# Optimization experiments

Hardware: AMD Instinct MI355X
Metric: run time of the kernel (lower is better)

Reference implementation:

```python
import jax, jax.numpy as jnp
import numpy as np

B, F, E = 16384, 50, 64          # batch, field_size, embedding_size
V, D = 100000, 512               # feature_size, deep_init_size
H1, H2 = 1024, 512               # deep_layers
BN_EPS = 1e-10


def setup_inputs() -> dict:
    key = jax.random.key(0)
    ks = jax.random.split(key, 14)
    g0 = np.sqrt(6.0 / (D + H1))
    g1 = np.sqrt(6.0 / (H1 + H2))
    go = np.sqrt(5.0 / (D + 1))
    return {
        "feat_index": jax.random.randint(ks[0], (B, F), 0, V),
        "feat_value": jax.random.uniform(ks[1], (B, F), dtype=jnp.float32),
        "feature_embeddings": jax.random.normal(ks[2], (V, E), dtype=jnp.float32) * 0.01,
        "product_linear": jax.random.normal(ks[3], (D, F, E), dtype=jnp.float32) * 0.01,
        "product_bias": jax.random.normal(ks[4], (D,), dtype=jnp.float32),
        "product_quadratic_inner": jax.random.normal(ks[5], (D, F), dtype=jnp.float32) * 0.01,
        "layer_0": jax.random.uniform(ks[6], (D, H1), minval=-g0, maxval=g0, dtype=jnp.float32),
        "bias_0": jax.random.uniform(ks[7], (1, H1), minval=-g0, maxval=g0, dtype=jnp.float32),
        "layer_1": jax.random.uniform(ks[8], (H1, H2), minval=-g1, maxval=g1, dtype=jnp.float32),
        "bias_1": jax.random.uniform(ks[9], (1, H2), minval=-g1, maxval=g1, dtype=jnp.float32),
        "bn_scale": jax.random.normal(ks[10], (1,), dtype=jnp.float32) * 0.01,
        "bn_offset": jax.random.normal(ks[11], (1,), dtype=jnp.float32) * 0.01,
        "output_w": jax.random.uniform(ks[12], (H2, 1), minval=-go, maxval=go, dtype=jnp.float32),
        "output_b": jnp.float32(0.01),
    }


def reference(feat_index, feat_value, feature_embeddings, product_linear,
              product_bias, product_quadratic_inner, layer_0, bias_0,
              layer_1, bias_1, bn_scale, bn_offset, output_w, output_b):
    # embedding lookup scaled by feature values: (B, F, E)
    emb = feature_embeddings[feat_index] * feat_value[..., None]
    # linear product signal: sum over field+embed dims for each of D units
    lz = jnp.einsum('bfe,dfe->bd', emb, product_linear)          # (B, D)
    # inner quadratic signal: field-weighted sum then L2 norm over embed dim
    s = jnp.einsum('bfe,df->bde', emb, product_quadratic_inner)  # (B, D, E)
    lp = jnp.sqrt(jnp.sum(s * s, axis=-1))                       # (B, D)
    y = jax.nn.relu(lz + lp + product_bias)
    # dropout omitted (deterministic eval-mode reference)
    for W, bvec in ((layer_0, bias_0), (layer_1, bias_1)):
        y = y @ W + bvec
        m = jnp.mean(y, axis=0)
        v = jnp.var(y, axis=0)
        y = (y - m) * jax.lax.rsqrt(v + BN_EPS) * bn_scale + bn_offset
        y = jax.nn.relu(y)
    out = y @ output_w + output_b
    return jax.nn.sigmoid(out)
```

## Files before the change

### kernel.cpp

```cpp
#include <hip/hip_runtime.h>

typedef unsigned short u16;
typedef __attribute__((ext_vector_type(8))) short bf16x8v;
typedef __attribute__((ext_vector_type(4))) float f32x4v;

#define B_SZ 16384
#define F_SZ 50
#define E_SZ 64
#define D_SZ 512
#define H1_SZ 1024
#define H2_SZ 512
#define KL 3200
#define KG 1280

__device__ __forceinline__ float b2f(u16 u){
  union { unsigned int i; float f; } v; v.i = ((unsigned int)u) << 16; return v.f;
}
__device__ __forceinline__ u16 f2b(float f){
  union { float f; unsigned int i; } v; v.f = f;
  unsigned int r = v.i + 0x7FFFu + ((v.i >> 16) & 1u);
  return (u16)(r >> 16);
}

__device__ __forceinline__ void gload16(const u16* g, u16* lds_base_uniform){
#if __has_builtin(__builtin_amdgcn_global_load_lds)
  __builtin_amdgcn_global_load_lds(
      (const __attribute__((address_space(1))) unsigned int*)g,
      (__attribute__((address_space(3))) unsigned int*)lds_base_uniform,
      16, 0, 0);
#else
  int lane = threadIdx.x & 63;
  *(uint4*)(lds_base_uniform + lane*8) = *(const uint4*)g;
#endif
}

__device__ __forceinline__ void swz(int id, int nblog2, int &x, int &y){
  int xcd = id & 7, j = id >> 3;
  x = j & ((1 << nblog2) - 1);
  y = ((j >> nblog2) << 3) | xcd;
}

__global__ __launch_bounds__(256) void k_gather(
    const int* __restrict__ fidx, const float* __restrict__ fval,
    const float* __restrict__ femb, u16* __restrict__ embT,
    u16* __restrict__ Gp)
{
  __shared__ int   sidx[F_SZ];
  __shared__ float sfv[F_SZ];
  __shared__ __align__(16) u16 tile[64*72];
  const int b = blockIdx.x, t = threadIdx.x;
  const int wave = t >> 6, lane = t & 63, quad = lane >> 4, l16 = lane & 15;
  if (t < F_SZ){ sidx[t] = fidx[b*F_SZ+t]; sfv[t] = fval[b*F_SZ+t]; }
  __syncthreads();
  #pragma unroll
  for (int i=0;i<4;i++){
    int k4 = (i*256+t)*4;
    if (k4 < F_SZ*E_SZ){
      int f = k4>>6, e = k4&63;
      float4 v = *(const float4*)&femb[(size_t)sidx[f]*E_SZ + e];
      float s = sfv[f];
      tile[f*72+e+0] = f2b(v.x*s);
      tile[f*72+e+1] = f2b(v.y*s);
      tile[f*72+e+2] = f2b(v.z*s);
      tile[f*72+e+3] = f2b(v.w*s);
    }
  }
  __syncthreads();
  u16* orow = embT + (size_t)b*KL;
  #pragma unroll
  for (int i=0;i<2;i++){
    int k8 = (i*256+t)*8;
    if (k8 < F_SZ*E_SZ){
      int f = k8>>6, e0 = k8&63;
      *(uint4*)&orow[k8] = *(const uint4*)&tile[f*72+e0];
    }
  }
  u16* grow = Gp + (size_t)b*KG;
  static const int TM[10] = {0,0,0,0,1,1,1,2,2,3};
  static const int TN[10] = {0,1,2,3,1,2,3,2,3,3};
  for (int ti = wave; ti < 10; ti += 4){
    const int tm = TM[ti], tn = TN[ti];
    f32x4v g = {0.f,0.f,0.f,0.f};
    #pragma unroll
    for (int ks=0;ks<2;ks++){
      bf16x8v af = *(const bf16x8v*)&tile[(tm*16+l16)*72 + (ks*4+quad)*8];
      bf16x8v bf = *(const bf16x8v*)&tile[(tn*16+l16)*72 + (ks*4+quad)*8];
      g = __builtin_amdgcn_mfma_f32_16x16x32_bf16(af, bf, g, 0, 0, 0);
    }
    const int gn = tn*16 + l16;
    #pragma unroll
    for (int r=0;r<4;r++){
      const int gm = tm*16 + quad*4 + r;
      if (gm < F_SZ && gn < F_SZ && gn >= gm)
        grow[gm*F_SZ - ((gm*(gm-1))>>1) + (gn-gm)] = f2b(g[r]);
    }
  }
  if (t < 5) grow[1275+t] = 0;
}

__global__ __launch_bounds__(256) void k_prep(
    const float* __restrict__ Wl, u16* __restrict__ WlT,
    const float* __restrict__ Pq, u16* __restrict__ pqq,
    const float* __restrict__ w0, u16* __restrict__ w0T,
    const float* __restrict__ w1, u16* __restrict__ w1T,
    const float* __restrict__ pb, const float* __restrict__ b0,
    float* __restrict__ cvec)
{
  const int r = blockIdx.x, t = threadIdx.x;
  if (r < 512){
    const int d = r;
    #pragma unroll
    for (int i=0;i<4;i++){
      int k4 = (i*256+t)*4;
      if (k4 < KL){
        float4 v = *(const float4*)&Wl[(size_t)d*KL + k4];
        u16* o = &WlT[(size_t)d*KL + k4];
        o[0]=f2b(v.x); o[1]=f2b(v.y); o[2]=f2b(v.z); o[3]=f2b(v.w);
      }
    }
  } else if (r < 1024){
    const int d = r - 512;
    const float* prow = &Pq[d*F_SZ];
    u16* orow = &pqq[(size_t)d*KG];
    int trif = 0;
    for (int f=0; f<F_SZ; f++){
      int len = F_SZ - f;
      if (t < len)
        orow[trif + t] = f2b(prow[f]*prow[f+t]*(t ? 2.f : 1.f));
      trif += len;
    }
    if (t < 5) orow[1275+t] = 0;
  } else if (r < 3072){
    int idx = (r-1024)*256 + t;
    int k = idx & 511, n = idx >> 9;
    w0T[idx] = f2b(w0[(size_t)k*H1_SZ + n]);
  } else if (r < 5120){
    int idx = (r-3072)*256 + t;
    int k = idx & 1023, n = idx >> 10;
    w1T[idx] = f2b(w1[(size_t)k*H2_SZ + n]);
  } else {
    int rr = r - 5120;
    int h = (rr & 3)*256 + t;
    int d0 = (rr >> 2)*64;
    float acc = (d0 == 0) ? b0[h] : 0.f;
    #pragma unroll 8
    for (int d=0; d<64; d++) acc += pb[d0+d]*w0[(size_t)(d0+d)*H1_SZ + h];
    atomicAdd(&cvec[h], acc);
  }
}


__global__ __launch_bounds__(256) void k_prod(
    const u16* __restrict__ Ae,
    const u16* __restrict__ Bw,
    const u16* __restrict__ Ag,
    const u16* __restrict__ Bq,
    const float* __restrict__ pbias,
    u16* __restrict__ y0)
{
  __shared__ __align__(16) u16 As[64*128];
  __shared__ __align__(16) u16 Bs[128*128];
  const int tid  = threadIdx.x;
  const int wave = tid >> 6, lane = tid & 63;
  const int quad = lane >> 4, l16 = lane & 15;
  int bx, by;  swz(blockIdx.x, 2, bx, by);
  const int n0 = bx * 128, m0 = by * 64;
  const int wr = wave >> 1, wc = wave & 1;
  const int lr4 = lane >> 4;
  const int cb  = lane & 15;
  const int sw  = (l16 & 7);

  f32x4v acc1[2][4], acc2[2][4];
  #pragma unroll
  for (int i=0;i<2;i++)
    #pragma unroll
    for (int j=0;j<4;j++){
      acc1[i][j] = (f32x4v){0.f,0.f,0.f,0.f};
      acc2[i][j] = (f32x4v){0.f,0.f,0.f,0.f};
    }

  auto run = [&](const u16* Ap, const u16* Bp, int K, f32x4v (&acc)[2][4]){
    for (int k0 = 0; k0 < K; k0 += 128){
      __syncthreads();
      #pragma unroll
      for (int c=0;c<4;c++){
        const int r0 = wave*16 + c*4;
        const int row = r0 + lr4;
        gload16(Ap + (size_t)(m0 + row)*K + k0 + ((cb ^ (row & 7)) << 3), As + r0*128);
      }
      #pragma unroll
      for (int c=0;c<8;c++){
        const int r0 = wave*32 + c*4;
        const int row = r0 + lr4;
        gload16(Bp + (size_t)(n0 + row)*K + k0 + ((cb ^ (row & 7)) << 3), Bs + r0*128);
      }
      __syncthreads();
      #pragma unroll
      for (int ks=0; ks<4; ks++){
        bf16x8v af[2], bfr[4];
        #pragma unroll
        for (int mt=0;mt<2;mt++)
          af[mt] = *(const bf16x8v*)&As[(wr*32+mt*16+l16)*128 + (((ks*4+quad) ^ sw))*8];
        #pragma unroll
        for (int nt=0;nt<4;nt++)
          bfr[nt] = *(const bf16x8v*)&Bs[(wc*64+nt*16+l16)*128 + (((ks*4+quad) ^ sw))*8];
        #pragma unroll
        for (int mt=0;mt<2;mt++)
          #pragma unroll
          for (int nt=0;nt<4;nt++)
            acc[mt][nt] = __builtin_amdgcn_mfma_f32_16x16x32_bf16(af[mt], bfr[nt], acc[mt][nt], 0, 0, 0);
      }
    }
  };

  run(Ae, Bw, KL, acc1);
  run(Ag, Bq, KG, acc2);

  #pragma unroll
  for (int nt=0;nt<4;nt++){
    const int n = n0 + wc*64 + nt*16 + l16;
    const float bv = pbias[n];
    #pragma unroll
    for (int mt=0;mt<2;mt++){
      const int mb = m0 + wr*32 + mt*16 + quad*4;
      #pragma unroll
      for (int r=0;r<4;r++){
        float v = acc1[mt][nt][r] + sqrtf(fmaxf(acc2[mt][nt][r], 0.f)) + bv;
        v = (v > 0.f ? v : 0.f) - bv;
        y0[(size_t)(mb+r)*D_SZ + n] = f2b(v);
      }
    }
  }
}

template<int DO_STATS, int CENTER, typename CT>
__global__ __launch_bounds__(256) void gemm_bt(
    const u16* __restrict__ A, const u16* __restrict__ Bm,
    CT* __restrict__ C, const float* __restrict__ bias,
    float* __restrict__ S1, float* __restrict__ S2,
    int nblog2, int N, int K)
{
  __shared__ __align__(16) u16 As[64*128];
  __shared__ __align__(16) u16 Bs[128*128];
  const int tid  = threadIdx.x;
  const int wave = tid >> 6, lane = tid & 63;
  const int quad = lane >> 4, l16 = lane & 15;
  int bx, by;  swz(blockIdx.x, nblog2, bx, by);
  const int n0 = bx * 128, m0 = by * 64;
  const int wr = wave >> 1, wc = wave & 1;
  const int lr4 = lane >> 4;
  const int cb  = lane & 15;
  const int sw  = (l16 & 7);

  f32x4v acc[2][4];
  #pragma unroll
  for (int i=0;i<2;i++)
    #pragma unroll
    for (int j=0;j<4;j++)
      acc[i][j] = (f32x4v){0.f,0.f,0.f,0.f};

  for (int k0 = 0; k0 < K; k0 += 128){
    __syncthreads();
    #pragma unroll
    for (int c=0;c<4;c++){
      const int r0 = wave*16 + c*4;
      const int row = r0 + lr4;
      gload16(A + (size_t)(m0 + row)*K + k0 + ((cb ^ (row & 7)) << 3), As + r0*128);
    }
    #pragma unroll
    for (int c=0;c<8;c++){
      const int r0 = wave*32 + c*4;
      const int row = r0 + lr4;
      gload16(Bm + (size_t)(n0 + row)*K + k0 + ((cb ^ (row & 7)) << 3), Bs + r0*128);
    }
    __syncthreads();
    #pragma unroll
    for (int ks=0; ks<4; ks++){
      bf16x8v af[2], bfr[4];
      #pragma unroll
      for (int mt=0;mt<2;mt++)
        af[mt] = *(const bf16x8v*)&As[(wr*32+mt*16+l16)*128 + (((ks*4+quad) ^ sw))*8];
      #pragma unroll
      for (int nt=0;nt<4;nt++)
        bfr[nt] = *(const bf16x8v*)&Bs[(wc*64+nt*16+l16)*128 + (((ks*4+quad) ^ sw))*8];
      #pragma unroll
      for (int mt=0;mt<2;mt++)
        #pragma unroll
        for (int nt=0;nt<4;nt++)
          acc[mt][nt] = __builtin_amdgcn_mfma_f32_16x16x32_bf16(af[mt], bfr[nt], acc[mt][nt], 0, 0, 0);
    }
  }

  #pragma unroll
  for (int nt=0;nt<4;nt++){
    const int n = n0 + wc*64 + nt*16 + l16;
    float bv = 0.f;
    if (DO_STATS) bv = bias[n];
    float ls1 = 0.f, ls2 = 0.f;
    #pragma unroll
    for (int mt=0;mt<2;mt++){
      const int mb = m0 + wr*32 + mt*16 + quad*4;
      #pragma unroll
      for (int r=0;r<4;r++){
        float v = acc[mt][nt][r] + bv;
        if constexpr (sizeof(CT) == 2) C[(size_t)(mb+r)*N + n] = f2b(CENTER ? acc[mt][nt][r] : v);
        else                           C[(size_t)(mb+r)*N + n] = v;
        ls1 += v; ls2 += v*v;
      }
    }
    if (DO_STATS){
      ls1 += __shfl_xor(ls1, 16); ls2 += __shfl_xor(ls2, 16);
      ls1 += __shfl_xor(ls1, 32); ls2 += __shfl_xor(ls2, 32);
      if (quad == 0){ atomicAdd(&S1[n], ls1); atomicAdd(&S2[n], ls2); }
    }
  }
}

__global__ void k_bnfin(const float* __restrict__ S1, const float* __restrict__ S2, int n,
                        const float* __restrict__ bnsc, const float* __restrict__ bnof,
                        const float* __restrict__ cadd,
                        float* __restrict__ Aout, float* __restrict__ Bout)
{
  int i = blockIdx.x*256 + threadIdx.x;
  if (i < n){
    const float invB = 1.f / 16384.f;
    float m   = S1[i]*invB;
    float var = S2[i]*invB - m*m;
    float a   = bnsc[0] * rsqrtf(var + 1e-10f);
    Aout[i] = a;
    Bout[i] = bnof[0] - m*a + a*cadd[i];
  }
}

__global__ __launch_bounds__(256) void k_bnapply(
    const u16* __restrict__ Z, u16* __restrict__ Y,
    const float* __restrict__ Aa, const float* __restrict__ Bb, int nmask)
{
  size_t base = ((size_t)blockIdx.x*256 + threadIdx.x) * 8;
  int n0 = (int)(base & (size_t)nmask);
  union { uint4 q; u16 s[8]; } z, o;
  z.q = *(const uint4*)&Z[base];
  #pragma unroll
  for (int j=0;j<8;j++){
    float v = b2f(z.s[j]) * Aa[n0+j] + Bb[n0+j];
    o.s[j] = f2b(v > 0.f ? v : 0.f);
  }
  *(uint4*)&Y[base] = o.q;
}

__global__ __launch_bounds__(256) void k_out(
    const u16* __restrict__ Z2, const float* __restrict__ wvec,
    const float* __restrict__ obp,
    const float* __restrict__ Aa, const float* __restrict__ Bb,
    float* __restrict__ out)
{
  const int wave = threadIdx.x >> 6, lane = threadIdx.x & 63;
  const int b = blockIdx.x*4 + wave;
  const int n0 = lane*8;
  union { uint4 q; u16 s[8]; } z;
  z.q = *(const uint4*)&Z2[(size_t)b*H2_SZ + n0];
  float4 wa = *(const float4*)&wvec[n0];
  float4 wb = *(const float4*)&wvec[n0+4];
  float wv[8] = {wa.x,wa.y,wa.z,wa.w,wb.x,wb.y,wb.z,wb.w};
  float s = 0.f;
  #pragma unroll
  for (int j=0;j<8;j++){
    float y = b2f(z.s[j]) * Aa[n0+j] + Bb[n0+j];
    y = y > 0.f ? y : 0.f;
    s += y * wv[j];
  }
  s += __shfl_xor(s,1);  s += __shfl_xor(s,2);  s += __shfl_xor(s,4);
  s += __shfl_xor(s,8);  s += __shfl_xor(s,16); s += __shfl_xor(s,32);
  if (lane == 0){
    float x = s + obp[0];
    out[b] = 1.f / (1.f + expf(-x));
  }
}


extern "C" void kernel_launch(void* const* d_in, const int* in_sizes, int n_in,
                              void* d_out, int out_size, void* d_ws, size_t ws_size,
                              hipStream_t stream)
{
  const int*   fidx  = (const int*)d_in[0];
  const float* fval  = (const float*)d_in[1];
  const float* femb  = (const float*)d_in[2];
  const float* wl    = (const float*)d_in[3];
  const float* pbias = (const float*)d_in[4];
  const float* pq    = (const float*)d_in[5];
  const float* w0    = (const float*)d_in[6];
  const float* b0    = (const float*)d_in[7];
  const float* w1    = (const float*)d_in[8];
  const float* b1    = (const float*)d_in[9];
  const float* bnsc  = (const float*)d_in[10];
  const float* bnof  = (const float*)d_in[11];
  const float* ow    = (const float*)d_in[12];
  const float* ob    = (const float*)d_in[13];
  float* out = (float*)d_out;

  char* ws = (char*)d_ws;
  u16*   embT = (u16*)(ws + 0);
  u16*   z1b  = (u16*)(ws + 0);
  u16*   y1b  = (u16*)(ws + 67108864);
  u16*   z2b  = (u16*)(ws + 100663296);
  u16*   gpb  = (u16*)(ws + 104857600);
  u16*   wlT  = (u16*)(ws + 146800640);
  u16*   pqqb = (u16*)(ws + 150077440);
  u16*   y0b  = (u16*)(ws + 151388160);
  u16*   w0T  = (u16*)(ws + 168165376);
  u16*   w1T  = (u16*)(ws + 169213952);
  float* S1a  = (float*)(ws + 170262528);
  float* S2a  = S1a + 1024;
  float* S1b  = S2a + 1024;
  float* S2b  = S1b + 512;
  float* cvec = S2b + 512;
  float* A0   = cvec + 1024;
  float* B0   = A0 + 1024;
  float* A1   = B0 + 1024;
  float* B1   = A1 + 512;

  hipMemsetAsync((void*)S1a, 0, 16384, stream);

  k_gather<<<B_SZ, 256, 0, stream>>>(fidx, fval, femb, embT, gpb);
  k_prep<<<5152, 256, 0, stream>>>(wl, wlT, pq, pqqb, w0, w0T, w1, w1T,
                                   pbias, b0, cvec);

  k_prod<<<1024, 256, 0, stream>>>(embT, wlT, gpb, pqqb, pbias, y0b);

  gemm_bt<1,1,u16><<<2048, 256, 0, stream>>>(y0b, w0T, z1b, cvec, S1a, S2a,
                                             3, H1_SZ, D_SZ);
  k_bnfin<<<4, 256, 0, stream>>>(S1a, S2a, 1024, bnsc, bnof, cvec, A0, B0);
  k_bnapply<<<8192, 256, 0, stream>>>(z1b, y1b, A0, B0, 1023);

  gemm_bt<1,1,u16><<<1024, 256, 0, stream>>>(y1b, w1T, z2b, b1, S1b, S2b,
                                             2, H2_SZ, H1_SZ);
  k_bnfin<<<2, 256, 0, stream>>>(S1b, S2b, 512, bnsc, bnof, b1, A1, B1);

  k_out<<<4096, 256, 0, stream>>>(z2b, ow, ob, A1, B1, out);
}
```

Before: 362.2 us.

## Merge gather and prep kernels, enlarge prod tile, fold BN finalize into consumers

Merges the embedding gather/Gram kernel and the weight-prep kernel into a single launch. The Gram triangle is now staged in LDS and written out with vector stores. The product GEMM tile grows from 64x128 to 128x128 per block, with each wave covering a full 32x128 strip and a 2-wave occupancy hint. The two small BN-finalize kernels are removed, and the BN scale and offset are recomputed per element inside bnapply and the output kernel. This cuts launch overhead and raises data reuse in the product GEMM, at the cost of more registers per thread, fewer blocks, and redundant rsqrt work.

```diff
diff --git a/kernel.cpp b/kernel.cpp
--- a/kernel.cpp
+++ b/kernel.cpp
@@ -40,65 +40,10 @@
   y = ((j >> nblog2) << 3) | xcd;
 }
 
-__global__ __launch_bounds__(256) void k_gather(
+__global__ __launch_bounds__(256) void k_front(
     const int* __restrict__ fidx, const float* __restrict__ fval,
     const float* __restrict__ femb, u16* __restrict__ embT,
-    u16* __restrict__ Gp)
-{
-  __shared__ int   sidx[F_SZ];
-  __shared__ float sfv[F_SZ];
-  __shared__ __align__(16) u16 tile[64*72];
-  const int b = blockIdx.x, t = threadIdx.x;
-  const int wave = t >> 6, lane = t & 63, quad = lane >> 4, l16 = lane & 15;
-  if (t < F_SZ){ sidx[t] = fidx[b*F_SZ+t]; sfv[t] = fval[b*F_SZ+t]; }
-  __syncthreads();
-  #pragma unroll
-  for (int i=0;i<4;i++){
-    int k4 = (i*256+t)*4;
-    if (k4 < F_SZ*E_SZ){
-      int f = k4>>6, e = k4&63;
-      float4 v = *(const float4*)&femb[(size_t)sidx[f]*E_SZ + e];
-      float s = sfv[f];
-      tile[f*72+e+0] = f2b(v.x*s);
-      tile[f*72+e+1] = f2b(v.y*s);
-      tile[f*72+e+2] = f2b(v.z*s);
-      tile[f*72+e+3] = f2b(v.w*s);
-    }
-  }
-  __syncthreads();
-  u16* orow = embT + (size_t)b*KL;
-  #pragma unroll
-  for (int i=0;i<2;i++){
-    int k8 = (i*256+t)*8;
-    if (k8 < F_SZ*E_SZ){
-      int f = k8>>6, e0 = k8&63;
-      *(uint4*)&orow[k8] = *(const uint4*)&tile[f*72+e0];
-    }
-  }
-  u16* grow = Gp + (size_t)b*KG;
-  static const int TM[10] = {0,0,0,0,1,1,1,2,2,3};
-  static const int TN[10] = {0,1,2,3,1,2,3,2,3,3};
-  for (int ti = wave; ti < 10; ti += 4){
-    const int tm = TM[ti], tn = TN[ti];
-    f32x4v g = {0.f,0.f,0.f,0.f};
-    #pragma unroll
-    for (int ks=0;ks<2;ks++){
-      bf16x8v af = *(const bf16x8v*)&tile[(tm*16+l16)*72 + (ks*4+quad)*8];
-      bf16x8v bf = *(const bf16x8v*)&tile[(tn*16+l16)*72 + (ks*4+quad)*8];
-      g = __builtin_amdgcn_mfma_f32_16x16x32_bf16(af, bf, g, 0, 0, 0);
-    }
-    const int gn = tn*16 + l16;
-    #pragma unroll
-    for (int r=0;r<4;r++){
-      const int gm = tm*16 + quad*4 + r;
-      if (gm < F_SZ && gn < F_SZ && gn >= gm)
-        grow[gm*F_SZ - ((gm*(gm-1))>>1) + (gn-gm)] = f2b(g[r]);
-    }
-  }
-  if (t < 5) grow[1275+t] = 0;
-}
-
-__global__ __launch_bounds__(256) void k_prep(
+    u16* __restrict__ Gp,
     const float* __restrict__ Wl, u16* __restrict__ WlT,
     const float* __restrict__ Pq, u16* __restrict__ pqq,
     const float* __restrict__ w0, u16* __restrict__ w0T,
@@ -106,9 +51,64 @@
     const float* __restrict__ pb, const float* __restrict__ b0,
     float* __restrict__ cvec)
 {
+  __shared__ int   sidx[F_SZ];
+  __shared__ float sfv[F_SZ];
+  __shared__ __align__(16) u16 tile[64*72];
+  __shared__ __align__(16) u16 gbuf[KG];
   const int r = blockIdx.x, t = threadIdx.x;
-  if (r < 512){
-    const int d = r;
+  if (r < 16384){
+    const int b = r;
+    const int wave = t >> 6, lane = t & 63, quad = lane >> 4, l16 = lane & 15;
+    if (t < F_SZ){ sidx[t] = fidx[b*F_SZ+t]; sfv[t] = fval[b*F_SZ+t]; }
+    if (t < 5) gbuf[1275+t] = 0;
+    __syncthreads();
+    #pragma unroll
+    for (int i=0;i<4;i++){
+      int k4 = (i*256+t)*4;
+      if (k4 < F_SZ*E_SZ){
+        int f = k4>>6, e = k4&63;
+        float4 v = *(const float4*)&femb[(size_t)sidx[f]*E_SZ + e];
+        float s = sfv[f];
+        tile[f*72+e+0] = f2b(v.x*s);
+        tile[f*72+e+1] = f2b(v.y*s);
+        tile[f*72+e+2] = f2b(v.z*s);
+        tile[f*72+e+3] = f2b(v.w*s);
+      }
+    }
+    __syncthreads();
+    u16* orow = embT + (size_t)b*KL;
+    #pragma unroll
+    for (int i=0;i<2;i++){
+      int k8 = (i*256+t)*8;
+      if (k8 < F_SZ*E_SZ){
+        int f = k8>>6, e0 = k8&63;
+        *(uint4*)&orow[k8] = *(const uint4*)&tile[f*72+e0];
+      }
+    }
+    static const int TM[10] = {0,0,0,0,1,1,1,2,2,3};
+    static const int TN[10] = {0,1,2,3,1,2,3,2,3,3};
+    for (int ti = wave; ti < 10; ti += 4){
+      const int tm = TM[ti], tn = TN[ti];
+      f32x4v g = {0.f,0.f,0.f,0.f};
+      #pragma unroll
+      for (int ks=0;ks<2;ks++){
+        bf16x8v af = *(const bf16x8v*)&tile[(tm*16+l16)*72 + (ks*4+quad)*8];
+        bf16x8v bf = *(const bf16x8v*)&tile[(tn*16+l16)*72 + (ks*4+quad)*8];
+        g = __builtin_amdgcn_mfma_f32_16x16x32_bf16(af, bf, g, 0, 0, 0);
+      }
+      const int gn = tn*16 + l16;
+      #pragma unroll
+      for (int rr=0;rr<4;rr++){
+        const int gm = tm*16 + quad*4 + rr;
+        if (gm < F_SZ && gn < F_SZ && gn >= gm)
+          gbuf[gm*F_SZ - ((gm*(gm-1))>>1) + (gn-gm)] = f2b(g[rr]);
+      }
+    }
+    __syncthreads();
+    if (t < 160)
+      *(uint4*)&Gp[(size_t)b*KG + t*8] = *(const uint4*)&gbuf[t*8];
+  } else if (r < 16896){
+    const int d = r - 16384;
     #pragma unroll
     for (int i=0;i<4;i++){
       int k4 = (i*256+t)*4;
@@ -118,8 +118,8 @@
         o[0]=f2b(v.x); o[1]=f2b(v.y); o[2]=f2b(v.z); o[3]=f2b(v.w);
       }
     }
-  } else if (r < 1024){
-    const int d = r - 512;
+  } else if (r < 17408){
+    const int d = r - 16896;
     const float* prow = &Pq[d*F_SZ];
     u16* orow = &pqq[(size_t)d*KG];
     int trif = 0;
@@ -130,16 +130,16 @@
       trif += len;
     }
     if (t < 5) orow[1275+t] = 0;
-  } else if (r < 3072){
-    int idx = (r-1024)*256 + t;
+  } else if (r < 19456){
+    int idx = (r-17408)*256 + t;
     int k = idx & 511, n = idx >> 9;
     w0T[idx] = f2b(w0[(size_t)k*H1_SZ + n]);
-  } else if (r < 5120){
-    int idx = (r-3072)*256 + t;
+  } else if (r < 21504){
+    int idx = (r-19456)*256 + t;
     int k = idx & 1023, n = idx >> 10;
     w1T[idx] = f2b(w1[(size_t)k*H2_SZ + n]);
   } else {
-    int rr = r - 5120;
+    int rr = r - 21504;
     int h = (rr & 3)*256 + t;
     int d0 = (rr >> 2)*64;
     float acc = (d0 == 0) ? b0[h] : 0.f;
@@ -150,7 +150,7 @@
 }
 
 
-__global__ __launch_bounds__(256) void k_prod(
+__global__ __launch_bounds__(256, 2) void k_prod(
     const u16* __restrict__ Ae,
     const u16* __restrict__ Bw,
     const u16* __restrict__ Ag,
@@ -158,33 +158,32 @@
     const float* __restrict__ pbias,
     u16* __restrict__ y0)
 {
-  __shared__ __align__(16) u16 As[64*128];
+  __shared__ __align__(16) u16 As[128*128];
   __shared__ __align__(16) u16 Bs[128*128];
   const int tid  = threadIdx.x;
   const int wave = tid >> 6, lane = tid & 63;
   const int quad = lane >> 4, l16 = lane & 15;
   int bx, by;  swz(blockIdx.x, 2, bx, by);
-  const int n0 = bx * 128, m0 = by * 64;
-  const int wr = wave >> 1, wc = wave & 1;
+  const int n0 = bx * 128, m0 = by * 128;
   const int lr4 = lane >> 4;
   const int cb  = lane & 15;
   const int sw  = (l16 & 7);
 
-  f32x4v acc1[2][4], acc2[2][4];
+  f32x4v acc1[2][8], acc2[2][8];
   #pragma unroll
   for (int i=0;i<2;i++)
     #pragma unroll
-    for (int j=0;j<4;j++){
+    for (int j=0;j<8;j++){
       acc1[i][j] = (f32x4v){0.f,0.f,0.f,0.f};
       acc2[i][j] = (f32x4v){0.f,0.f,0.f,0.f};
     }
 
-  auto run = [&](const u16* Ap, const u16* Bp, int K, f32x4v (&acc)[2][4]){
+  auto run = [&](const u16* Ap, const u16* Bp, int K, f32x4v (&acc)[2][8]){
     for (int k0 = 0; k0 < K; k0 += 128){
       __syncthreads();
       #pragma unroll
-      for (int c=0;c<4;c++){
-        const int r0 = wave*16 + c*4;
+      for (int c=0;c<8;c++){
+        const int r0 = wave*32 + c*4;
         const int row = r0 + lr4;
         gload16(Ap + (size_t)(m0 + row)*K + k0 + ((cb ^ (row & 7)) << 3), As + r0*128);
       }
@@ -197,17 +196,17 @@
       __syncthreads();
       #pragma unroll
       for (int ks=0; ks<4; ks++){
-        bf16x8v af[2], bfr[4];
+        bf16x8v af[2], bfr[8];
         #pragma unroll
         for (int mt=0;mt<2;mt++)
-          af[mt] = *(const bf16x8v*)&As[(wr*32+mt*16+l16)*128 + (((ks*4+quad) ^ sw))*8];
+          af[mt] = *(const bf16x8v*)&As[(wave*32+mt*16+l16)*128 + (((ks*4+quad) ^ sw))*8];
         #pragma unroll
-        for (int nt=0;nt<4;nt++)
-          bfr[nt] = *(const bf16x8v*)&Bs[(wc*64+nt*16+l16)*128 + (((ks*4+quad) ^ sw))*8];
+        for (int nt=0;nt<8;nt++)
+          bfr[nt] = *(const bf16x8v*)&Bs[(nt*16+l16)*128 + (((ks*4+quad) ^ sw))*8];
         #pragma unroll
         for (int mt=0;mt<2;mt++)
           #pragma unroll
-          for (int nt=0;nt<4;nt++)
+          for (int nt=0;nt<8;nt++)
             acc[mt][nt] = __builtin_amdgcn_mfma_f32_16x16x32_bf16(af[mt], bfr[nt], acc[mt][nt], 0, 0, 0);
       }
     }
@@ -217,12 +216,12 @@
   run(Ag, Bq, KG, acc2);
 
   #pragma unroll
-  for (int nt=0;nt<4;nt++){
-    const int n = n0 + wc*64 + nt*16 + l16;
+  for (int nt=0;nt<8;nt++){
+    const int n = n0 + nt*16 + l16;
     const float bv = pbias[n];
     #pragma unroll
     for (int mt=0;mt<2;mt++){
-      const int mb = m0 + wr*32 + mt*16 + quad*4;
+      const int mb = m0 + wave*32 + mt*16 + quad*4;
       #pragma unroll
       for (int r=0;r<4;r++){
         float v = acc1[mt][nt][r] + sqrtf(fmaxf(acc2[mt][nt][r], 0.f)) + bv;
@@ -316,33 +315,26 @@
   }
 }
 
-__global__ void k_bnfin(const float* __restrict__ S1, const float* __restrict__ S2, int n,
-                        const float* __restrict__ bnsc, const float* __restrict__ bnof,
-                        const float* __restrict__ cadd,
-                        float* __restrict__ Aout, float* __restrict__ Bout)
-{
-  int i = blockIdx.x*256 + threadIdx.x;
-  if (i < n){
-    const float invB = 1.f / 16384.f;
-    float m   = S1[i]*invB;
-    float var = S2[i]*invB - m*m;
-    float a   = bnsc[0] * rsqrtf(var + 1e-10f);
-    Aout[i] = a;
-    Bout[i] = bnof[0] - m*a + a*cadd[i];
-  }
-}
-
 __global__ __launch_bounds__(256) void k_bnapply(
     const u16* __restrict__ Z, u16* __restrict__ Y,
-    const float* __restrict__ Aa, const float* __restrict__ Bb, int nmask)
+    const float* __restrict__ S1, const float* __restrict__ S2,
+    const float* __restrict__ bnsc, const float* __restrict__ bnof,
+    const float* __restrict__ cadd, int nmask)
 {
   size_t base = ((size_t)blockIdx.x*256 + threadIdx.x) * 8;
   int n0 = (int)(base & (size_t)nmask);
+  const float invB = 1.f / 16384.f;
+  const float sc = bnsc[0], of = bnof[0];
   union { uint4 q; u16 s[8]; } z, o;
   z.q = *(const uint4*)&Z[base];
   #pragma unroll
   for (int j=0;j<8;j++){
-    float v = b2f(z.s[j]) * Aa[n0+j] + Bb[n0+j];
+    int n = n0 + j;
+    float m   = S1[n]*invB;
+    float var = S2[n]*invB - m*m;
+    float a   = sc * rsqrtf(var + 1e-10f);
+    float bb  = of - m*a + a*cadd[n];
+    float v = b2f(z.s[j]) * a + bb;
     o.s[j] = f2b(v > 0.f ? v : 0.f);
   }
   *(uint4*)&Y[base] = o.q;
@@ -351,12 +343,16 @@
 __global__ __launch_bounds__(256) void k_out(
     const u16* __restrict__ Z2, const float* __restrict__ wvec,
     const float* __restrict__ obp,
-    const float* __restrict__ Aa, const float* __restrict__ Bb,
+    const float* __restrict__ S1, const float* __restrict__ S2,
+    const float* __restrict__ bnsc, const float* __restrict__ bnof,
+    const float* __restrict__ cadd,
     float* __restrict__ out)
 {
   const int wave = threadIdx.x >> 6, lane = threadIdx.x & 63;
   const int b = blockIdx.x*4 + wave;
   const int n0 = lane*8;
+  const float invB = 1.f / 16384.f;
+  const float sc = bnsc[0], of = bnof[0];
   union { uint4 q; u16 s[8]; } z;
   z.q = *(const uint4*)&Z2[(size_t)b*H2_SZ + n0];
   float4 wa = *(const float4*)&wvec[n0];
@@ -365,7 +361,12 @@
   float s = 0.f;
   #pragma unroll
   for (int j=0;j<8;j++){
-    float y = b2f(z.s[j]) * Aa[n0+j] + Bb[n0+j];
+    int n = n0 + j;
+    float m   = S1[n]*invB;
+    float var = S2[n]*invB - m*m;
+    float a   = sc * rsqrtf(var + 1e-10f);
+    float bb  = of - m*a + a*cadd[n];
+    float y = b2f(z.s[j]) * a + bb;
     y = y > 0.f ? y : 0.f;
     s += y * wv[j];
   }
@@ -414,27 +415,21 @@
   float* S1b  = S2a + 1024;
   float* S2b  = S1b + 512;
   float* cvec = S2b + 512;
-  float* A0   = cvec + 1024;
-  float* B0   = A0 + 1024;
-  float* A1   = B0 + 1024;
-  float* B1   = A1 + 512;
 
   hipMemsetAsync((void*)S1a, 0, 16384, stream);
 
-  k_gather<<<B_SZ, 256, 0, stream>>>(fidx, fval, femb, embT, gpb);
-  k_prep<<<5152, 256, 0, stream>>>(wl, wlT, pq, pqqb, w0, w0T, w1, w1T,
-                                   pbias, b0, cvec);
-
-  k_prod<<<1024, 256, 0, stream>>>(embT, wlT, gpb, pqqb, pbias, y0b);
+  k_front<<<21536, 256, 0, stream>>>(fidx, fval, femb, embT, gpb,
+                                     wl, wlT, pq, pqqb, w0, w0T, w1, w1T,
+                                     pbias, b0, cvec);
+
+  k_prod<<<512, 256, 0, stream>>>(embT, wlT, gpb, pqqb, pbias, y0b);
 
   gemm_bt<1,1,u16><<<2048, 256, 0, stream>>>(y0b, w0T, z1b, cvec, S1a, S2a,
                                              3, H1_SZ, D_SZ);
-  k_bnfin<<<4, 256, 0, stream>>>(S1a, S2a, 1024, bnsc, bnof, cvec, A0, B0);
-  k_bnapply<<<8192, 256, 0, stream>>>(z1b, y1b, A0, B0, 1023);
+  k_bnapply<<<8192, 256, 0, stream>>>(z1b, y1b, S1a, S2a, bnsc, bnof, cvec, 1023);
 
   gemm_bt<1,1,u16><<<1024, 256, 0, stream>>>(y1b, w1T, z2b, b1, S1b, S2b,
                                              2, H2_SZ, H1_SZ);
-  k_bnfin<<<2, 256, 0, stream>>>(S1b, S2b, 512, bnsc, bnof, b1, A1, B1);
-
-  k_out<<<4096, 256, 0, stream>>>(z2b, ow, ob, A1, B1, out);
-}
+
+  k_out<<<4096, 256, 0, stream>>>(z2b, ow, ob, S1b, S2b, bnsc, bnof, b1, out);
+}
```

New measurement: 326.6 us. 1.11x faster.
